# Kernel tuning notes

Measured on AMD Instinct MI355X. Metric: run time of the kernel, lower is better.

Reference implementation:

```python
import jax, jax.numpy as jnp
import numpy as np

ALPHA = 1.702
LIMIT = 7.0
EPS = 1e-5

E, K, H, I = 8, 2, 2048, 2048
B, S = 1, 1024


def setup_inputs() -> dict:
    key = jax.random.key(0)
    k1, k2, k3, k4, k5 = jax.random.split(key, 5)
    x = jax.random.normal(k1, (B, S, H), dtype=jnp.float32)
    norm_w = jax.random.normal(k2, (H,), dtype=jnp.float32) * 0.02 + 1.0
    router_w = jax.random.normal(k3, (E, H), dtype=jnp.float32) * (1.0 / np.sqrt(H))
    w_gu = jax.random.normal(k4, (E, H, 2 * I), dtype=jnp.float32) * (1.0 / np.sqrt(H))
    w_down = jax.random.normal(k5, (E, I, H), dtype=jnp.float32) * (1.0 / np.sqrt(I))
    return {"x": x, "norm_w": norm_w, "router_w": router_w,
            "w_gu": w_gu, "w_down": w_down, "top_k": K}


def _rmsnorm(x, w):
    var = jnp.mean(x * x, axis=-1, keepdims=True)
    return x * jax.lax.rsqrt(var + EPS) * w


def _swiglu(h):
    # interleaved gate/linear halves, clamped (GPT-OSS style)
    glu = jnp.minimum(h[..., ::2], LIMIT)
    lin = jnp.clip(h[..., 1::2], -LIMIT, LIMIT)
    return glu * jax.nn.sigmoid(ALPHA * glu) * (lin + 1.0)


def reference(x, norm_w, router_w, w_gu, w_down, top_k):
    b, s, h = x.shape
    t = _rmsnorm(x, norm_w).reshape(b * s, h)          # [T, H]
    T = t.shape[0]

    # Router: linear -> softmax -> top-k -> normalize selected affinities
    logits = jnp.einsum('th,eh->te', t, router_w)      # [T, E]
    probs = jax.nn.softmax(logits, axis=-1)
    vals, idx = jax.lax.top_k(probs, top_k)            # [T, K]
    vals = vals / jnp.sum(vals, axis=-1, keepdims=True)
    cw = jnp.zeros_like(probs).at[jnp.arange(T)[:, None], idx].add(vals)  # [T, E]

    # Expert MLPs (dense per-expert reference of the blockwise grouped GEMM)
    hgu = jnp.einsum('th,ehf->etf', t, w_gu)           # [E, T, 2I]
    act = _swiglu(hgu)                                 # [E, T, I]
    oe = jnp.einsum('eti,eio->eto', act, w_down)       # [E, T, H]
    out = jnp.einsum('eto,te->to', oe, cw)             # [T, H]
    return out.reshape(b, s, h)
```

## Files before the change

kernel.cpp:

```cpp
#include <hip/hip_runtime.h>
#include <hip/hip_bf16.h>

#define H_   2048
#define E_   8
#define T_   1024
#define TWOI 4096
#define I_   2048
#define ALPHA 1.702f
#define LIMIT 7.0f

#define BM 128
#define BN 128
#define BKK 32
#define BTW 40

typedef __attribute__((ext_vector_type(8))) short short8;
typedef __attribute__((ext_vector_type(4))) float f32x4;

#define AS3U(p) ((__attribute__((address_space(3))) unsigned int*)(p))
#define AS1U(p) ((const __attribute__((address_space(1))) unsigned int*)(p))

__device__ __forceinline__ unsigned short f2bf(float f) {
    unsigned int u = __float_as_uint(f);
    u += 0x7fff + ((u >> 16) & 1);
    return (unsigned short)(u >> 16);
}

__device__ __forceinline__ unsigned int cvtpk_bf16(float lo, float hi) {
    unsigned int r;
    asm("v_cvt_pk_bf16_f32 %0, %1, %2" : "=v"(r) : "v"(lo), "v"(hi));
    return r;
}

__global__ void zero_kernel(float* __restrict__ out, int n, int* __restrict__ counts) {
    int i = blockIdx.x * blockDim.x + threadIdx.x;
    if (i < n) out[i] = 0.0f;
    if (i < E_) counts[i] = 0;
}

__global__ __launch_bounds__(256) void rms_router(
    const float* __restrict__ x, const float* __restrict__ nw,
    const float* __restrict__ rw,
    unsigned short* __restrict__ tbf, int* __restrict__ counts,
    int* __restrict__ tlist, float* __restrict__ tw)
{
    int t = blockIdx.x;
    int tid = threadIdx.x;
    int wave = tid >> 6, lane = tid & 63;
    const float* xr = x + (size_t)t * H_;

    float4 v0 = *(const float4*)(xr + tid * 4);
    float4 v1 = *(const float4*)(xr + 1024 + tid * 4);
    float ss = v0.x*v0.x + v0.y*v0.y + v0.z*v0.z + v0.w*v0.w
             + v1.x*v1.x + v1.y*v1.y + v1.z*v1.z + v1.w*v1.w;
    #pragma unroll
    for (int s = 32; s; s >>= 1) ss += __shfl_xor(ss, s);

    __shared__ float red[4];
    __shared__ float wlog[4][8];
    if (lane == 0) red[wave] = ss;
    __syncthreads();
    float total = red[0] + red[1] + red[2] + red[3];
    float scale = rsqrtf(total * (1.0f / H_) + 1e-5f);

    float4 n0 = *(const float4*)(nw + tid * 4);
    float4 n1 = *(const float4*)(nw + 1024 + tid * 4);
    float tv[8];
    tv[0] = v0.x * scale * n0.x; tv[1] = v0.y * scale * n0.y;
    tv[2] = v0.z * scale * n0.z; tv[3] = v0.w * scale * n0.w;
    tv[4] = v1.x * scale * n1.x; tv[5] = v1.y * scale * n1.y;
    tv[6] = v1.z * scale * n1.z; tv[7] = v1.w * scale * n1.w;

    ushort4 o0 = make_ushort4(f2bf(tv[0]), f2bf(tv[1]), f2bf(tv[2]), f2bf(tv[3]));
    ushort4 o1 = make_ushort4(f2bf(tv[4]), f2bf(tv[5]), f2bf(tv[6]), f2bf(tv[7]));
    *(ushort4*)(tbf + (size_t)t * H_ + tid * 4) = o0;
    *(ushort4*)(tbf + (size_t)t * H_ + 1024 + tid * 4) = o1;

    float acc[E_];
    #pragma unroll
    for (int e = 0; e < E_; e++) {
        const float* r0 = rw + (size_t)e * H_ + tid * 4;
        float4 a = *(const float4*)r0;
        float4 b = *(const float4*)(r0 + 1024);
        acc[e] = tv[0]*a.x + tv[1]*a.y + tv[2]*a.z + tv[3]*a.w
               + tv[4]*b.x + tv[5]*b.y + tv[6]*b.z + tv[7]*b.w;
    }
    #pragma unroll
    for (int s = 32; s; s >>= 1)
        #pragma unroll
        for (int e = 0; e < E_; e++) acc[e] += __shfl_xor(acc[e], s);
    if (lane == 0)
        #pragma unroll
        for (int e = 0; e < E_; e++) wlog[wave][e] = acc[e];
    __syncthreads();

    if (tid == 0) {
        float lg[E_];
        #pragma unroll
        for (int e = 0; e < E_; e++)
            lg[e] = wlog[0][e] + wlog[1][e] + wlog[2][e] + wlog[3][e];
        int i0 = 0;
        #pragma unroll
        for (int e = 1; e < E_; e++) if (lg[e] > lg[i0]) i0 = e;
        int i1 = -1;
        #pragma unroll
        for (int e = 0; e < E_; e++) {
            if (e == i0) continue;
            if (i1 < 0 || lg[e] > lg[i1]) i1 = e;
        }
        float e1 = expf(lg[i1] - lg[i0]);
        float s = 1.0f + e1;
        float w0 = 1.0f / s, w1 = e1 / s;
        int p0 = atomicAdd(&counts[i0], 1);
        tlist[i0 * T_ + p0] = t; tw[i0 * T_ + p0] = w0;
        int p1 = atomicAdd(&counts[i1], 1);
        tlist[i1 * T_ + p1] = t; tw[i1 * T_ + p1] = w1;
    }
}

__device__ __forceinline__ void compute_step(
    const unsigned short (*Asb)[BKK], const unsigned short (*Btb)[BTW],
    int wm, int wn, int lane, f32x4 acc[4][4])
{
    short8 a[4], b[4];
    int arow = wm * 64 + (lane & 15);
    int brow = wn * 64 + (lane & 15);
    int koff = (lane >> 4) * 8;
    #pragma unroll
    for (int mi = 0; mi < 4; mi++)
        a[mi] = *(const short8*)(&Asb[arow + mi * 16][koff]);
    #pragma unroll
    for (int ni = 0; ni < 4; ni++)
        b[ni] = *(const short8*)(&Btb[brow + ni * 16][koff]);
    #pragma unroll
    for (int mi = 0; mi < 4; mi++)
        #pragma unroll
        for (int ni = 0; ni < 4; ni++)
            acc[mi][ni] = __builtin_amdgcn_mfma_f32_16x16x32_bf16(a[mi], b[ni], acc[mi][ni], 0, 0, 0);
}

#define STEP(TT, RCUR, RNEXT, PRE) {                                               \
    if (PRE) {                                                                     \
        int kk2_ = ((TT) + 2) * BKK;                                               \
        __builtin_amdgcn_global_load_lds(AS1U(asrc0 + kk2_), AS3U(&As[c2][wave * 32][0]), 16, 0, 0);      \
        __builtin_amdgcn_global_load_lds(AS1U(asrc1 + kk2_), AS3U(&As[c2][wave * 32 + 16][0]), 16, 0, 0); \
        _Pragma("unroll")                                                          \
        for (int j = 0; j < 16; j++)                                               \
            RNEXT[j] = bcol[(size_t)(kk2_ + sk + j) * ldbv];                       \
    }                                                                              \
    compute_step(As[c0], Bt[(TT) & 1], wm, wn, lane, acc);                         \
    {                                                                              \
        unsigned int pk_[8];                                                       \
        _Pragma("unroll")                                                          \
        for (int h = 0; h < 8; h++) pk_[h] = cvtpk_bf16(RCUR[2 * h], RCUR[2 * h + 1]); \
        unsigned short* db_ = &Bt[((TT) + 1) & 1][sn][sk];                         \
        *(uint4*)(db_)     = make_uint4(pk_[0], pk_[1], pk_[2], pk_[3]);           \
        *(uint4*)(db_ + 8) = make_uint4(pk_[4], pk_[5], pk_[6], pk_[7]);           \
    }                                                                              \
    if (PRE) { asm volatile("s_waitcnt vmcnt(18)" ::: "memory"); }                 \
    else     { asm volatile("s_waitcnt vmcnt(0)"  ::: "memory"); }                 \
    asm volatile("s_waitcnt lgkmcnt(0)" ::: "memory");                             \
    __builtin_amdgcn_sched_barrier(0);                                             \
    __builtin_amdgcn_s_barrier();                                                  \
    __builtin_amdgcn_sched_barrier(0);                                             \
    { int tmp_ = c0; c0 = c1; c1 = c2; c2 = tmp_; }                                \
}

#define GEMM_PIPELINE(NS)                                                          \
    float r0[16], r1[16];                                                          \
    int c0 = 0, c1 = 1, c2 = 2;                                                    \
                                    \
    __builtin_amdgcn_global_load_lds(AS1U(asrc0), AS3U(&As[0][wave * 32][0]), 16, 0, 0);            \
    __builtin_amdgcn_global_load_lds(AS1U(asrc1), AS3U(&As[0][wave * 32 + 16][0]), 16, 0, 0);       \
    _Pragma("unroll")                                                              \
    for (int j = 0; j < 16; j++) r0[j] = bcol[(size_t)(sk + j) * ldbv];            \
    __builtin_amdgcn_global_load_lds(AS1U(asrc0 + BKK), AS3U(&As[1][wave * 32][0]), 16, 0, 0);      \
    __builtin_amdgcn_global_load_lds(AS1U(asrc1 + BKK), AS3U(&As[1][wave * 32 + 16][0]), 16, 0, 0); \
    _Pragma("unroll")                                                              \
    for (int j = 0; j < 16; j++) r1[j] = bcol[(size_t)(BKK + sk + j) * ldbv];      \
    {                                                                              \
        unsigned int pk_[8];                                                       \
        _Pragma("unroll")                                                          \
        for (int h = 0; h < 8; h++) pk_[h] = cvtpk_bf16(r0[2 * h], r0[2 * h + 1]); \
        unsigned short* db_ = &Bt[0][sn][sk];                                      \
        *(uint4*)(db_)     = make_uint4(pk_[0], pk_[1], pk_[2], pk_[3]);           \
        *(uint4*)(db_ + 8) = make_uint4(pk_[4], pk_[5], pk_[6], pk_[7]);           \
    }                                                                              \
    asm volatile("s_waitcnt vmcnt(18)" ::: "memory");                              \
    asm volatile("s_waitcnt lgkmcnt(0)" ::: "memory");                             \
    __builtin_amdgcn_sched_barrier(0);                                             \
    __builtin_amdgcn_s_barrier();                                                  \
    __builtin_amdgcn_sched_barrier(0);                                             \
    for (int t = 0; t < (NS) - 2; t += 2) {                                        \
        STEP(t,     r1, r0, 1)                                                     \
        STEP(t + 1, r0, r1, 1)                                                     \
    }                                                                              \
    STEP((NS) - 2, r1, r0, 0)                                                      \
    compute_step(As[c0], Bt[((NS) - 1) & 1], wm, wn, lane, acc);

__global__ __launch_bounds__(256, 3) void gu_gemm(
    const unsigned short* __restrict__ tbf,
    const float* __restrict__ wgu,
    const int* __restrict__ counts, const int* __restrict__ tlist,
    unsigned short* __restrict__ act)
{
    int bid = blockIdx.x;
    int mtile = bid >> 8;
    int rem = bid & 255;
    int e = rem >> 5;
    int n0 = (rem & 31) * BN;

    int cnt = counts[e];
    int m0 = mtile * BM;
    if (m0 >= cnt) return;

    __shared__ __align__(16) unsigned short As[3][BM][BKK];
    __shared__ __align__(16) unsigned short Bt[2][BN][BTW];

    int tid = threadIdx.x;
    int lane = tid & 63, wave = tid >> 6;
    int wm = wave >> 1, wn = wave & 1;

    int row0 = wave * 32 + (lane >> 2);
    int gr0 = m0 + row0, gr1 = gr0 + 16;
    int tok0 = tlist[e * T_ + (gr0 < cnt ? gr0 : 0)];
    int tok1 = tlist[e * T_ + (gr1 < cnt ? gr1 : 0)];
    const unsigned short* asrc0 = tbf + (size_t)tok0 * H_ + (lane & 3) * 8;
    const unsigned short* asrc1 = tbf + (size_t)tok1 * H_ + (lane & 3) * 8;

    int sn = tid & 127;
    int sk = (tid >> 7) * 16;
    const float* bcol = wgu + (size_t)e * H_ * TWOI + n0 + sn;
    const int ldbv = TWOI;

    f32x4 acc[4][4];
    #pragma unroll
    for (int mi = 0; mi < 4; mi++)
        #pragma unroll
        for (int ni = 0; ni < 4; ni++) acc[mi][ni] = (f32x4){0.f, 0.f, 0.f, 0.f};

    GEMM_PIPELINE(64)

    #pragma unroll
    for (int mi = 0; mi < 4; mi++) {
        #pragma unroll
        for (int ni = 0; ni < 4; ni++) {
            #pragma unroll
            for (int r = 0; r < 4; r++) {
                float v = acc[mi][ni][r];
                float p = __shfl_xor(v, 1);
                int rowe = wm * 64 + mi * 16 + (lane >> 4) * 4 + r;
                int grow = m0 + rowe;
                if (!(lane & 1) && grow < cnt) {
                    float glu = fminf(v, LIMIT);
                    float lin = fminf(fmaxf(p, -LIMIT), LIMIT);
                    float g = glu / (1.0f + __expf(-ALPHA * glu));
                    float a_ = g * (lin + 1.0f);
                    int col = n0 + wn * 64 + ni * 16 + (lane & 15);
                    act[((size_t)e * T_ + grow) * I_ + (col >> 1)] = f2bf(a_);
                }
            }
        }
    }
}

__global__ __launch_bounds__(256, 3) void down_gemm(
    const unsigned short* __restrict__ act,
    const float* __restrict__ wdn,
    const int* __restrict__ counts, const int* __restrict__ tlist,
    const float* __restrict__ tw, float* __restrict__ out)
{
    int bid = blockIdx.x;
    int mtile = bid >> 8;
    int rem = bid & 255;
    int e = rem >> 5;
    int ks = (rem >> 4) & 1;
    int ntile = rem & 15;
    int n0 = ntile * BN;
    int kbase = ks * (I_ / 2);

    int cnt = counts[e];
    int m0 = mtile * BM;
    if (m0 >= cnt) return;

    __shared__ __align__(16) unsigned short As[3][BM][BKK];
    __shared__ __align__(16) unsigned short Bt[2][BN][BTW];

    int tid = threadIdx.x;
    int lane = tid & 63, wave = tid >> 6;
    int wm = wave >> 1, wn = wave & 1;

    int row0 = wave * 32 + (lane >> 2);
    const unsigned short* asrc0 = act + ((size_t)e * T_ + m0 + row0) * I_ + kbase + (lane & 3) * 8;
    const unsigned short* asrc1 = asrc0 + (size_t)16 * I_;

    int sn = tid & 127;
    int sk = (tid >> 7) * 16;
    const float* bcol = wdn + (size_t)e * I_ * H_ + (size_t)kbase * H_ + n0 + sn;
    const int ldbv = H_;

    f32x4 acc[4][4];
    #pragma unroll
    for (int mi = 0; mi < 4; mi++)
        #pragma unroll
        for (int ni = 0; ni < 4; ni++) acc[mi][ni] = (f32x4){0.f, 0.f, 0.f, 0.f};

    GEMM_PIPELINE(32)

    #pragma unroll
    for (int mi = 0; mi < 4; mi++) {
        #pragma unroll
        for (int ni = 0; ni < 4; ni++) {
            #pragma unroll
            for (int r = 0; r < 4; r++) {
                int rowe = wm * 64 + mi * 16 + (lane >> 4) * 4 + r;
                int grow = m0 + rowe;
                if (grow < cnt) {
                    int tok = tlist[e * T_ + grow];
                    float w = tw[e * T_ + grow];
                    int col = n0 + wn * 64 + ni * 16 + (lane & 15);
                    atomicAdd(&out[(size_t)tok * H_ + col], w * acc[mi][ni][r]);
                }
            }
        }
    }
}

extern "C" void kernel_launch(void* const* d_in, const int* in_sizes, int n_in,
                              void* d_out, int out_size, void* d_ws, size_t ws_size,
                              hipStream_t stream)
{
    const float* x   = (const float*)d_in[0];
    const float* nw  = (const float*)d_in[1];
    const float* rw  = (const float*)d_in[2];
    const float* wgu = (const float*)d_in[3];
    const float* wdn = (const float*)d_in[4];
    float* out = (float*)d_out;

    char* ws = (char*)d_ws;
    unsigned short* tbf = (unsigned short*)ws;
    unsigned short* act = (unsigned short*)(ws + (4u << 20));
    int*   counts = (int*)(ws + (36u << 20));
    int*   tlist  = (int*)(ws + (36u << 20) + 256);
    float* tw     = (float*)(ws + (36u << 20) + 256 + 8 * 1024 * 4);

    int n = T_ * H_;
    zero_kernel<<<dim3((n + 255) / 256), 256, 0, stream>>>(out, n, counts);
    rms_router<<<dim3(T_), 256, 0, stream>>>(x, nw, rw, tbf, counts, tlist, tw);
    gu_gemm<<<dim3(2048), 256, 0, stream>>>(tbf, wgu, counts, tlist, act);
    down_gemm<<<dim3(2048), 256, 0, stream>>>(act, wdn, counts, tlist, tw, out);
}
```

Before: 207.5 us.

## Replace atomic output scatter with per-slot partial buffers and a combine pass

```diff
diff --git a/kernel.cpp b/kernel.cpp
--- a/kernel.cpp
+++ b/kernel.cpp
@@ -32,9 +32,8 @@
     return r;
 }
 
-__global__ void zero_kernel(float* __restrict__ out, int n, int* __restrict__ counts) {
-    int i = blockIdx.x * blockDim.x + threadIdx.x;
-    if (i < n) out[i] = 0.0f;
+__global__ void zero_counts(int* __restrict__ counts) {
+    int i = threadIdx.x;
     if (i < E_) counts[i] = 0;
 }
 
@@ -42,7 +41,7 @@
     const float* __restrict__ x, const float* __restrict__ nw,
     const float* __restrict__ rw,
     unsigned short* __restrict__ tbf, int* __restrict__ counts,
-    int* __restrict__ tlist, float* __restrict__ tw)
+    int* __restrict__ tlist, int* __restrict__ tslot, float* __restrict__ tw)
 {
     int t = blockIdx.x;
     int tid = threadIdx.x;
@@ -112,9 +111,9 @@
         float s = 1.0f + e1;
         float w0 = 1.0f / s, w1 = e1 / s;
         int p0 = atomicAdd(&counts[i0], 1);
-        tlist[i0 * T_ + p0] = t; tw[i0 * T_ + p0] = w0;
+        tlist[i0 * T_ + p0] = t; tslot[i0 * T_ + p0] = 0; tw[i0 * T_ + p0] = w0;
         int p1 = atomicAdd(&counts[i1], 1);
-        tlist[i1 * T_ + p1] = t; tw[i1 * T_ + p1] = w1;
+        tlist[i1 * T_ + p1] = t; tslot[i1 * T_ + p1] = 1; tw[i1 * T_ + p1] = w1;
     }
 }
 
@@ -268,7 +267,8 @@
     const unsigned short* __restrict__ act,
     const float* __restrict__ wdn,
     const int* __restrict__ counts, const int* __restrict__ tlist,
-    const float* __restrict__ tw, float* __restrict__ out)
+    const int* __restrict__ tslot, const float* __restrict__ tw,
+    float* __restrict__ parts)
 {
     int bid = blockIdx.x;
     int mtile = bid >> 8;
@@ -309,21 +309,41 @@
 
     #pragma unroll
     for (int mi = 0; mi < 4; mi++) {
-        #pragma unroll
-        for (int ni = 0; ni < 4; ni++) {
-            #pragma unroll
-            for (int r = 0; r < 4; r++) {
-                int rowe = wm * 64 + mi * 16 + (lane >> 4) * 4 + r;
-                int grow = m0 + rowe;
-                if (grow < cnt) {
-                    int tok = tlist[e * T_ + grow];
-                    float w = tw[e * T_ + grow];
+        int rowe = wm * 64 + mi * 16 + (lane >> 4) * 4;
+        int grow0 = m0 + rowe;
+        #pragma unroll
+        for (int r = 0; r < 4; r++) {
+            int grow = grow0 + r;
+            if (grow < cnt) {
+                int tok  = tlist[e * T_ + grow];
+                int slot = tslot[e * T_ + grow];
+                float w  = tw[e * T_ + grow];
+                float* dst = parts + ((size_t)(ks * 2 + slot) * T_ + tok) * H_;
+                #pragma unroll
+                for (int ni = 0; ni < 4; ni++) {
                     int col = n0 + wn * 64 + ni * 16 + (lane & 15);
-                    atomicAdd(&out[(size_t)tok * H_ + col], w * acc[mi][ni][r]);
+                    dst[col] = w * acc[mi][ni][r];
                 }
             }
         }
     }
+}
+
+__global__ __launch_bounds__(256) void combine_kernel(
+    const float* __restrict__ parts, float* __restrict__ out)
+{
+    int i = blockIdx.x * blockDim.x + threadIdx.x;
+    const float4* p0 = (const float4*)parts;
+    const float4* p1 = (const float4*)(parts + (size_t)T_ * H_);
+    const float4* p2 = (const float4*)(parts + (size_t)2 * T_ * H_);
+    const float4* p3 = (const float4*)(parts + (size_t)3 * T_ * H_);
+    float4 a = p0[i], b = p1[i], c = p2[i], d = p3[i];
+    float4 s;
+    s.x = (a.x + b.x) + (c.x + d.x);
+    s.y = (a.y + b.y) + (c.y + d.y);
+    s.z = (a.z + b.z) + (c.z + d.z);
+    s.w = (a.w + b.w) + (c.w + d.w);
+    ((float4*)out)[i] = s;
 }
 
 extern "C" void kernel_launch(void* const* d_in, const int* in_sizes, int n_in,
@@ -340,13 +360,15 @@
     char* ws = (char*)d_ws;
     unsigned short* tbf = (unsigned short*)ws;
     unsigned short* act = (unsigned short*)(ws + (4u << 20));
-    int*   counts = (int*)(ws + (36u << 20));
-    int*   tlist  = (int*)(ws + (36u << 20) + 256);
-    float* tw     = (float*)(ws + (36u << 20) + 256 + 8 * 1024 * 4);
-
-    int n = T_ * H_;
-    zero_kernel<<<dim3((n + 255) / 256), 256, 0, stream>>>(out, n, counts);
-    rms_router<<<dim3(T_), 256, 0, stream>>>(x, nw, rw, tbf, counts, tlist, tw);
+    float* parts = (float*)(ws + (36u << 20));
+    int*   counts = (int*)(ws + (68u << 20));
+    int*   tlist  = (int*)(ws + (68u << 20) + 256);
+    int*   tslot  = (int*)(ws + (68u << 20) + 256 + 32 * 1024);
+    float* tw     = (float*)(ws + (68u << 20) + 256 + 64 * 1024);
+
+    zero_counts<<<dim3(1), 64, 0, stream>>>(counts);
+    rms_router<<<dim3(T_), 256, 0, stream>>>(x, nw, rw, tbf, counts, tlist, tslot, tw);
     gu_gemm<<<dim3(2048), 256, 0, stream>>>(tbf, wgu, counts, tlist, act);
-    down_gemm<<<dim3(2048), 256, 0, stream>>>(act, wdn, counts, tlist, tw, out);
-}
+    down_gemm<<<dim3(2048), 256, 0, stream>>>(act, wdn, counts, tlist, tslot, tw, parts);
+    combine_kernel<<<dim3((T_ * H_ / 4) / 256), 256, 0, stream>>>(parts, out);
+}
```

Result: faster. 189.3 us (-8.8%).
